# Kernel tuning notes

Measured on AMD Instinct MI355X. Metric: run time of the kernel, lower is better.

## Reference

```python
import jax, jax.numpy as jnp
import numpy as np

N_NODES = 100000
N_EDGES = 1600000
N_GRAPHS = 1024
IN_CH = 64
HID = 32
H4, H2 = HID * 4, HID * 2


def _glorot(key, shape):
    fan_in, fan_out = shape[0], shape[1]
    lim = (6.0 / (fan_in + fan_out)) ** 0.5
    return jax.random.uniform(key, shape, jnp.float32, -lim, lim)


def setup_inputs() -> dict:
    key = jax.random.key(0)
    ks = jax.random.split(key, 32)
    inp = {
        "x": jax.random.normal(ks[0], (N_NODES, IN_CH), jnp.float32),
        "edge_index": jax.random.randint(ks[1], (2, N_EDGES), 0, N_NODES, jnp.int64),
        "batch": jnp.sort(jax.random.randint(ks[2], (N_NODES,), 0, N_GRAPHS, jnp.int64)),
    }
    dims = [(IN_CH, H4), (H4, H2), (H2, H2), (H2, H2)]
    for i, (di, do) in enumerate(dims, 1):
        inp[f"c{i}_wl"] = _glorot(ks[3 * i], (di, do))
        inp[f"c{i}_bl"] = jnp.zeros((do,), jnp.float32)
        inp[f"c{i}_wr"] = _glorot(ks[3 * i + 1], (di, do))
    lin_dims = [(H2, H2), (H2, HID), (HID, HID), (HID, 1)]
    for i, (di, do) in enumerate(lin_dims, 1):
        inp[f"lin{i}_w"] = _glorot(ks[15 + 2 * i], (di, do))
        inp[f"lin{i}_b"] = jnp.zeros((do,), jnp.float32)
    return inp


def _sage(x, src, dst, wl, bl, wr):
    # mean-aggregate neighbor (source) features at target nodes
    agg = jax.ops.segment_sum(x[src], dst, num_segments=N_NODES)
    deg = jax.ops.segment_sum(jnp.ones((src.shape[0],), x.dtype), dst, num_segments=N_NODES)
    agg = agg / jnp.maximum(deg, 1.0)[:, None]
    return agg @ wl + bl + x @ wr


def reference(x, edge_index, batch,
              c1_wl, c1_bl, c1_wr, c2_wl, c2_bl, c2_wr,
              c3_wl, c3_bl, c3_wr, c4_wl, c4_bl, c4_wr,
              lin1_w, lin1_b, lin2_w, lin2_b, lin3_w, lin3_b, lin4_w, lin4_b):
    src, dst = edge_index[0], edge_index[1]
    h = jax.nn.relu(_sage(x, src, dst, c1_wl, c1_bl, c1_wr))
    h = jax.nn.relu(_sage(h, src, dst, c2_wl, c2_bl, c2_wr))
    h = jax.nn.relu(_sage(h, src, dst, c3_wl, c3_bl, c3_wr))
    h = jax.nn.relu(_sage(h, src, dst, c4_wl, c4_bl, c4_wr))
    # global mean pool over graphs
    gsum = jax.ops.segment_sum(h, batch, num_segments=N_GRAPHS)
    gcnt = jax.ops.segment_sum(jnp.ones((h.shape[0],), h.dtype), batch, num_segments=N_GRAPHS)
    g = gsum / jnp.maximum(gcnt, 1.0)[:, None]
    g = jax.nn.relu(g @ lin1_w + lin1_b)
    g = jax.nn.relu(g @ lin2_w + lin2_b)
    g = jax.nn.relu(g @ lin3_w + lin3_b)
    out = (g @ lin4_w + lin4_b).squeeze(1)  # [N_GRAPHS]
    return out
```

## Files before the change

### kernel.cpp

```cpp
#include <hip/hip_runtime.h>

#define NN 100000
#define NE 1600000
#define NG 1024
#define NBLK_SCAN ((NN + 255) / 256)
#define NPART 2
#define CPAD 4

#define GB_COUNT 6250
#define GB_Z     1563
#define GB_CVT   3125
#define GB_BND   5
#define GB_PREP  320
#define GB_SETUP (2 * GB_COUNT)

typedef __attribute__((ext_vector_type(8))) short bf16x8;
typedef __attribute__((ext_vector_type(4))) float f32x4;

__device__ __forceinline__ unsigned f2bf1(float f) {
  union { float f; unsigned u; } v; v.f = f;
  return (v.u + 0x7fffu + ((v.u >> 16) & 1u)) >> 16;
}
__device__ __forceinline__ unsigned packbf2(float a, float b) {
  return f2bf1(a) | (f2bf1(b) << 16);
}
__device__ __forceinline__ float bflo(unsigned u) {
  union { unsigned u; float f; } v; v.u = u << 16; return v.f;
}
__device__ __forceinline__ float bfhi(unsigned u) {
  union { unsigned u; float f; } v; v.u = u & 0xffff0000u; return v.f;
}
__device__ __forceinline__ float bfs(unsigned short s) {
  union { unsigned u; float f; } v; v.u = ((unsigned)s) << 16; return v.f;
}

__global__ __launch_bounds__(256) void k_prepz(const float* __restrict__ c1wr,
                                               unsigned short* __restrict__ pLZ) {
  int e = blockIdx.x * 256 + threadIdx.x;
  if (e >= 64 * 128) return;
  int k = e >> 7, n = e & 127;
  int t = k >> 5, kq = (k >> 3) & 3, j = k & 7;
  int n0 = n >> 4, nl = n & 15;
  pLZ[((((n0 * 2 + t) * 64) + (kq * 16 + nl)) << 3) + j] =
      (unsigned short)f2bf1(c1wr[k * 128 + n]);
}

__global__ __launch_bounds__(256) void k_setup(
    const int* __restrict__ dst, int* __restrict__ cnt, int* __restrict__ rank,
    const float* __restrict__ X, unsigned short* __restrict__ Xb,
    const int* __restrict__ batch, int* __restrict__ gstart,
    const unsigned short* __restrict__ pLZ, const float* __restrict__ c1bl,
    unsigned short* __restrict__ ZZ,
    const float* __restrict__ c1wl, const float* __restrict__ c1wr,
    const float* __restrict__ c2wl, const float* __restrict__ c2wr,
    const float* __restrict__ c3wl, const float* __restrict__ c3wr,
    const float* __restrict__ c4wl, const float* __restrict__ c4wr,
    unsigned short* __restrict__ pL1, unsigned short* __restrict__ pL2a,
    unsigned short* __restrict__ pL2b, unsigned short* __restrict__ pL3,
    unsigned short* __restrict__ pL4) {
  __shared__ __align__(16) char smem[64 * 66 * 4];
  int b = blockIdx.x, tid = threadIdx.x;

  if ((b & 1) == 0) {
    int e = (b >> 1) * 256 + tid;
    rank[e] = atomicAdd(&cnt[(size_t)dst[e] * CPAD], 1);
    return;
  }
  int ob = b >> 1;

  if (ob < GB_Z) {
    unsigned short* sA = (unsigned short*)smem;
    float* sC = (float*)smem;
    const int m0 = ob * 64;
#pragma unroll
    for (int l = 0; l < 2; ++l) {
      int c = tid + l * 256;
      int m = c >> 3, k8 = c & 7;
      int row = m0 + m;
      uint4 o = make_uint4(0, 0, 0, 0);
      if (row < NN) {
        const float4* xp = (const float4*)(X + (size_t)row * 64 + k8 * 8);
        float4 p0 = xp[0], p1 = xp[1];
        o.x = packbf2(p0.x, p0.y); o.y = packbf2(p0.z, p0.w);
        o.z = packbf2(p1.x, p1.y); o.w = packbf2(p1.z, p1.w);
      }
      int wv = m >> 4, mr = m & 15, t = k8 >> 2, kq = k8 & 3;
      ((uint4*)sA)[(wv * 2 + t) * 64 + kq * 16 + mr] = o;
    }
    __syncthreads();
    const int w = tid >> 6, L = tid & 63;
    const bf16x8* Af = (const bf16x8*)sA;
    const bf16x8* Bf = (const bf16x8*)pLZ;
    f32x4 acc[8];
#pragma unroll
    for (int i = 0; i < 8; ++i)
#pragma unroll
      for (int j = 0; j < 4; ++j) acc[i][j] = 0.f;
#pragma unroll
    for (int t = 0; t < 2; ++t) {
      bf16x8 afr = Af[(w * 2 + t) * 64 + L];
#pragma unroll
      for (int n0 = 0; n0 < 8; ++n0) {
        bf16x8 bfr = Bf[(n0 * 2 + t) * 64 + L];
        acc[n0] = __builtin_amdgcn_mfma_f32_16x16x32_bf16(afr, bfr, acc[n0], 0, 0, 0);
      }
    }
    int rg = L >> 4, cl = L & 15;
#pragma unroll
    for (int half = 0; half < 2; ++half) {
      __syncthreads();
#pragma unroll
      for (int n0 = 0; n0 < 4; ++n0)
#pragma unroll
        for (int r = 0; r < 4; ++r)
          sC[(w * 16 + rg * 4 + r) * 66 + n0 * 16 + cl] = acc[half * 4 + n0][r];
      __syncthreads();
#pragma unroll
      for (int it = 0; it < 2; ++it) {
        int c = tid + it * 256;
        int m = c >> 3, c8 = c & 7;
        int row = m0 + m;
        if (row < NN) {
          float v[8];
#pragma unroll
          for (int j = 0; j < 8; ++j)
            v[j] = sC[m * 66 + c8 * 8 + j] + c1bl[half * 64 + c8 * 8 + j];
          uint4 o;
          o.x = packbf2(v[0], v[1]); o.y = packbf2(v[2], v[3]);
          o.z = packbf2(v[4], v[5]); o.w = packbf2(v[6], v[7]);
          ((uint4*)(ZZ + (size_t)row * 128 + half * 64))[c8] = o;
        }
      }
    }
    return;
  }
  ob -= GB_Z;
  if (ob < GB_CVT) {
    int i = ob * 256 + tid;
    const float4* p = (const float4*)X + (size_t)i * 2;
    float4 a = p[0], c = p[1];
    uint4 o;
    o.x = packbf2(a.x, a.y); o.y = packbf2(a.z, a.w);
    o.z = packbf2(c.x, c.y); o.w = packbf2(c.z, c.w);
    ((uint4*)Xb)[i] = o;
    return;
  }
  ob -= GB_CVT;
  if (ob < GB_BND) {
    int g = ob * 256 + tid;
    if (g > NG) return;
    int lo = 0, hi = NN;
    while (lo < hi) {
      int mid = (lo + hi) >> 1;
      if (batch[mid] < g) lo = mid + 1; else hi = mid;
    }
    gstart[g] = lo;
    return;
  }
  ob -= GB_BND;
  if (ob < GB_PREP) {
    int yb = ob >> 6, xb = ob & 63;
    const float *WL, *WR; unsigned short* dstp; int N;
    if (yb == 0)      { WL = c1wl; WR = c1wr;           dstp = pL1;  N = 128; }
    else if (yb == 1) { WL = c2wl; WR = c2wl + 64 * 64; dstp = pL2a; N = 64; }
    else if (yb == 2) { WL = c2wr; WR = c2wr + 64 * 64; dstp = pL2b; N = 64; }
    else if (yb == 3) { WL = c3wl; WR = c3wr;           dstp = pL3;  N = 64; }
    else              { WL = c4wl; WR = c4wr;           dstp = pL4;  N = 64; }
    int e = xb * 256 + tid;
    if (e >= 128 * N) return;
    int k = e / N, n = e - k * N;
    float w = (k < 64) ? WL[k * N + n] : WR[(k - 64) * N + n];
    int t = k >> 5, kq = (k >> 3) & 3, j = k & 7;
    int n0 = n >> 4, nl = n & 15;
    dstp[((((n0 * 4 + t) * 64) + (kq * 16 + nl)) << 3) + j] =
        (unsigned short)f2bf1(w);
  }
}

__global__ __launch_bounds__(256) void k_scan1(const int* __restrict__ cnt,
                                               int* __restrict__ off,
                                               int* __restrict__ bsum) {
  __shared__ int s[256];
  int tid = threadIdx.x;
  int i = blockIdx.x * 256 + tid;
  int v = (i < NN) ? cnt[(size_t)i * CPAD] : 0;
  s[tid] = v;
  __syncthreads();
  for (int d = 1; d < 256; d <<= 1) {
    int t = (tid >= d) ? s[tid - d] : 0;
    __syncthreads();
    s[tid] += t;
    __syncthreads();
  }
  if (i < NN) off[i] = s[tid] - v;
  if (tid == 255) bsum[blockIdx.x] = s[255];
}

__global__ __launch_bounds__(256) void k_scan23(int* __restrict__ off,
                                                const int* __restrict__ bsum,
                                                const int* __restrict__ cnt,
                                                float* __restrict__ inv) {
  __shared__ int red[256];
  int b = blockIdx.x, tid = threadIdx.x;
  int s = 0;
  for (int j = tid; j < b; j += 256) s += bsum[j];
  red[tid] = s;
  __syncthreads();
  for (int d = 128; d > 0; d >>= 1) {
    if (tid < d) red[tid] += red[tid + d];
    __syncthreads();
  }
  int base = red[0];
  int i = b * 256 + tid;
  if (i < NN) {
    off[i] = off[i] + base;
    inv[i] = 1.0f / fmaxf((float)cnt[(size_t)i * CPAD], 1.0f);
  }
  if (i == 0) off[NN] = NE;
}

__global__ __launch_bounds__(256) void k_fill(const int* __restrict__ src,
                                              const int* __restrict__ dst,
                                              const int* __restrict__ off,
                                              const int* __restrict__ rank,
                                              int* __restrict__ csr) {
  int e = blockIdx.x * 256 + threadIdx.x;
  int lo = (int)blockIdx.y * (NN / NPART);
  int hi = lo + (NN / NPART);
  if (e < NE) {
    int d = dst[e];
    if (d >= lo && d < hi) csr[off[d] + rank[e]] = src[e];
  }
}

__global__ __launch_bounds__(256) void k_gather(
    const unsigned short* __restrict__ F, const int* __restrict__ csr,
    const int* __restrict__ off, const float* __restrict__ inv,
    const float* __restrict__ bias, const unsigned short* __restrict__ Z,
    unsigned short* __restrict__ out) {
  int idx = blockIdx.x * 256 + threadIdx.x;
  int n = idx >> 3, q = idx & 7;
  int beg = off[n], end = off[n + 1];
  float aA[8], aB[8];
#pragma unroll
  for (int c = 0; c < 8; ++c) { aA[c] = 0.f; aB[c] = 0.f; }
  int e = beg;
  for (; e + 4 <= end; e += 4) {
    uint4 v[4];
#pragma unroll
    for (int j = 0; j < 4; ++j)
      v[j] = ((const uint4*)(F + (size_t)csr[e + j] * 64))[q];
#pragma unroll
    for (int j = 0; j < 4; j += 2) {
      aA[0] += bflo(v[j].x); aB[0] += bflo(v[j + 1].x);
      aA[1] += bfhi(v[j].x); aB[1] += bfhi(v[j + 1].x);
      aA[2] += bflo(v[j].y); aB[2] += bflo(v[j + 1].y);
      aA[3] += bfhi(v[j].y); aB[3] += bfhi(v[j + 1].y);
      aA[4] += bflo(v[j].z); aB[4] += bflo(v[j + 1].z);
      aA[5] += bfhi(v[j].z); aB[5] += bfhi(v[j + 1].z);
      aA[6] += bflo(v[j].w); aB[6] += bflo(v[j + 1].w);
      aA[7] += bfhi(v[j].w); aB[7] += bfhi(v[j + 1].w);
    }
  }
  for (; e < end; ++e) {
    uint4 v0 = ((const uint4*)(F + (size_t)csr[e] * 64))[q];
    aA[0] += bflo(v0.x); aA[1] += bfhi(v0.x);
    aA[2] += bflo(v0.y); aA[3] += bfhi(v0.y);
    aA[4] += bflo(v0.z); aA[5] += bfhi(v0.z);
    aA[6] += bflo(v0.w); aA[7] += bfhi(v0.w);
  }
  float a[8];
  float iv = inv[n];
#pragma unroll
  for (int c = 0; c < 8; ++c) a[c] = (aA[c] + aB[c]) * iv;
  {
    uint4 z = ((const uint4*)(Z + (size_t)n * 64))[q];
    const float4* bp = (const float4*)(bias + q * 8);
    float4 b0 = bp[0], b1 = bp[1];
    a[0] = fmaxf(a[0] + b0.x + bflo(z.x), 0.f);
    a[1] = fmaxf(a[1] + b0.y + bfhi(z.x), 0.f);
    a[2] = fmaxf(a[2] + b0.z + bflo(z.y), 0.f);
    a[3] = fmaxf(a[3] + b0.w + bfhi(z.y), 0.f);
    a[4] = fmaxf(a[4] + b1.x + bflo(z.z), 0.f);
    a[5] = fmaxf(a[5] + b1.y + bfhi(z.z), 0.f);
    a[6] = fmaxf(a[6] + b1.z + bflo(z.w), 0.f);
    a[7] = fmaxf(a[7] + b1.w + bfhi(z.w), 0.f);
  }
  uint4 o;
  o.x = packbf2(a[0], a[1]); o.y = packbf2(a[2], a[3]);
  o.z = packbf2(a[4], a[5]); o.w = packbf2(a[6], a[7]);
  ((uint4*)(out + (size_t)n * 64))[q] = o;
}

__global__ __launch_bounds__(256, 4) void k_fgemm1(
    const unsigned short* __restrict__ F, const int* __restrict__ csr,
    const int* __restrict__ off, const float* __restrict__ inv,
    const unsigned short* __restrict__ Wp,
    const unsigned short* __restrict__ ZZ,
    unsigned short* __restrict__ OUT) {
  __shared__ __align__(16) char smem[64 * 66 * 4];
  unsigned short* sA = (unsigned short*)smem;
  float* sC = (float*)smem;
  const int tid = threadIdx.x;
  const int m0 = blockIdx.x * 64;

  {
    int m = tid >> 2, qr = tid & 3;
    int row = m0 + m;
    float a0[16], a1[16];
#pragma unroll
    for (int c = 0; c < 16; ++c) { a0[c] = 0.f; a1[c] = 0.f; }
    if (row < NN) {
      int beg = off[row], end = off[row + 1];
      int e = beg;
      for (; e + 2 <= end; e += 2) {
        int s0 = csr[e], s1 = csr[e + 1];
        const uint4* r0 = (const uint4*)(F + (size_t)s0 * 64) + qr * 2;
        const uint4* r1 = (const uint4*)(F + (size_t)s1 * 64) + qr * 2;
        uint4 p0 = r0[0], p1 = r0[1], q0 = r1[0], q1 = r1[1];
        a0[0] += bflo(p0.x); a0[1] += bfhi(p0.x);
        a0[2] += bflo(p0.y); a0[3] += bfhi(p0.y);
        a0[4] += bflo(p0.z); a0[5] += bfhi(p0.z);
        a0[6] += bflo(p0.w); a0[7] += bfhi(p0.w);
        a0[8] += bflo(p1.x); a0[9] += bfhi(p1.x);
        a0[10] += bflo(p1.y); a0[11] += bfhi(p1.y);
        a0[12] += bflo(p1.z); a0[13] += bfhi(p1.z);
        a0[14] += bflo(p1.w); a0[15] += bfhi(p1.w);
        a1[0] += bflo(q0.x); a1[1] += bfhi(q0.x);
        a1[2] += bflo(q0.y); a1[3] += bfhi(q0.y);
        a1[4] += bflo(q0.z); a1[5] += bfhi(q0.z);
        a1[6] += bflo(q0.w); a1[7] += bfhi(q0.w);
        a1[8] += bflo(q1.x); a1[9] += bfhi(q1.x);
        a1[10] += bflo(q1.y); a1[11] += bfhi(q1.y);
        a1[12] += bflo(q1.z); a1[13] += bfhi(q1.z);
        a1[14] += bflo(q1.w); a1[15] += bfhi(q1.w);
      }
      if (e < end) {
        const uint4* r0 = (const uint4*)(F + (size_t)csr[e] * 64) + qr * 2;
        uint4 p0 = r0[0], p1 = r0[1];
        a0[0] += bflo(p0.x); a0[1] += bfhi(p0.x);
        a0[2] += bflo(p0.y); a0[3] += bfhi(p0.y);
        a0[4] += bflo(p0.z); a0[5] += bfhi(p0.z);
        a0[6] += bflo(p0.w); a0[7] += bfhi(p0.w);
        a0[8] += bflo(p1.x); a0[9] += bfhi(p1.x);
        a0[10] += bflo(p1.y); a0[11] += bfhi(p1.y);
        a0[12] += bflo(p1.z); a0[13] += bfhi(p1.z);
        a0[14] += bflo(p1.w); a0[15] += bfhi(p1.w);
      }
      float iv = inv[row];
#pragma unroll
      for (int c = 0; c < 16; ++c) a0[c] = (a0[c] + a1[c]) * iv;
    }
    int wv = m >> 4, mr = m & 15;
#pragma unroll
    for (int h = 0; h < 2; ++h) {
      int k8 = qr * 2 + h;
      int t = k8 >> 2, kq = k8 & 3;
      uint4 o;
      o.x = packbf2(a0[h * 8 + 0], a0[h * 8 + 1]);
      o.y = packbf2(a0[h * 8 + 2], a0[h * 8 + 3]);
      o.z = packbf2(a0[h * 8 + 4], a0[h * 8 + 5]);
      o.w = packbf2(a0[h * 8 + 6], a0[h * 8 + 7]);
      ((uint4*)sA)[(wv * 2 + t) * 64 + kq * 16 + mr] = o;
    }
  }
  __syncthreads();

  const int w = tid >> 6, L = tid & 63;
  const bf16x8* Af = (const bf16x8*)sA;
  const bf16x8* Bf = (const bf16x8*)Wp;
  f32x4 acc[8];
#pragma unroll
  for (int i = 0; i < 8; ++i)
#pragma unroll
    for (int j = 0; j < 4; ++j) acc[i][j] = 0.f;
#pragma unroll
  for (int t = 0; t < 2; ++t) {
    bf16x8 afr = Af[(w * 2 + t) * 64 + L];
#pragma unroll
    for (int n0 = 0; n0 < 8; ++n0) {
      bf16x8 bfr = Bf[(n0 * 4 + t) * 64 + L];
      acc[n0] = __builtin_amdgcn_mfma_f32_16x16x32_bf16(afr, bfr, acc[n0], 0, 0, 0);
    }
  }

  int rg = L >> 4, cl = L & 15;
#pragma unroll
  for (int half = 0; half < 2; ++half) {
    __syncthreads();
#pragma unroll
    for (int n0 = 0; n0 < 4; ++n0)
#pragma unroll
      for (int r = 0; r < 4; ++r)
        sC[(w * 16 + rg * 4 + r) * 66 + n0 * 16 + cl] = acc[half * 4 + n0][r];
    __syncthreads();
#pragma unroll
    for (int it = 0; it < 2; ++it) {
      int c = tid + it * 256;
      int m = c >> 3, c8 = c & 7;
      int row = m0 + m;
      if (row < NN) {
        uint4 z = ((const uint4*)(ZZ + (size_t)row * 128 + half * 64))[c8];
        float zb[8] = {bflo(z.x), bfhi(z.x), bflo(z.y), bfhi(z.y),
                       bflo(z.z), bfhi(z.z), bflo(z.w), bfhi(z.w)};
        float v[8];
#pragma unroll
        for (int j = 0; j < 8; ++j)
          v[j] = fmaxf(sC[m * 66 + c8 * 8 + j] + zb[j], 0.f);
        uint4 o;
        o.x = packbf2(v[0], v[1]); o.y = packbf2(v[2], v[3]);
        o.z = packbf2(v[4], v[5]); o.w = packbf2(v[6], v[7]);
        ((uint4*)(OUT + (size_t)row * 128 + half * 64))[c8] = o;
      }
    }
  }
}

template <int NF>
__global__ __launch_bounds__(256, 4) void k_fgemm(
    const unsigned short* __restrict__ F, const int* __restrict__ csr,
    const int* __restrict__ off, const float* __restrict__ inv,
    const unsigned short* __restrict__ Wp, const float* __restrict__ bias,
    unsigned short* __restrict__ OUT, int outStride) {
  __shared__ __align__(16) char smem[64 * 66 * 4];
  unsigned short* sA = (unsigned short*)smem;
  float* sC = (float*)smem;
  const int tid = threadIdx.x;
  const int m0 = blockIdx.x * 64;

  {
    int m = tid >> 2, qr = tid & 3;
    int row = m0 + m;
    float a0[16], a1[16];
#pragma unroll
    for (int c = 0; c < 16; ++c) { a0[c] = 0.f; a1[c] = 0.f; }
    if (row < NN) {
      int beg = off[row], end = off[row + 1];
      int e = beg;
      for (; e + 2 <= end; e += 2) {
        int s0 = csr[e], s1 = csr[e + 1];
        const uint4* r0 = (const uint4*)(F + (size_t)s0 * 64) + qr * 2;
        const uint4* r1 = (const uint4*)(F + (size_t)s1 * 64) + qr * 2;
        uint4 p0 = r0[0], p1 = r0[1], q0 = r1[0], q1 = r1[1];
        a0[0] += bflo(p0.x); a0[1] += bfhi(p0.x);
        a0[2] += bflo(p0.y); a0[3] += bfhi(p0.y);
        a0[4] += bflo(p0.z); a0[5] += bfhi(p0.z);
        a0[6] += bflo(p0.w); a0[7] += bfhi(p0.w);
        a0[8] += bflo(p1.x); a0[9] += bfhi(p1.x);
        a0[10] += bflo(p1.y); a0[11] += bfhi(p1.y);
        a0[12] += bflo(p1.z); a0[13] += bfhi(p1.z);
        a0[14] += bflo(p1.w); a0[15] += bfhi(p1.w);
        a1[0] += bflo(q0.x); a1[1] += bfhi(q0.x);
        a1[2] += bflo(q0.y); a1[3] += bfhi(q0.y);
        a1[4] += bflo(q0.z); a1[5] += bfhi(q0.z);
        a1[6] += bflo(q0.w); a1[7] += bfhi(q0.w);
        a1[8] += bflo(q1.x); a1[9] += bfhi(q1.x);
        a1[10] += bflo(q1.y); a1[11] += bfhi(q1.y);
        a1[12] += bflo(q1.z); a1[13] += bfhi(q1.z);
        a1[14] += bflo(q1.w); a1[15] += bfhi(q1.w);
      }
      if (e < end) {
        const uint4* r0 = (const uint4*)(F + (size_t)csr[e] * 64) + qr * 2;
        uint4 p0 = r0[0], p1 = r0[1];
        a0[0] += bflo(p0.x); a0[1] += bfhi(p0.x);
        a0[2] += bflo(p0.y); a0[3] += bfhi(p0.y);
        a0[4] += bflo(p0.z); a0[5] += bfhi(p0.z);
        a0[6] += bflo(p0.w); a0[7] += bfhi(p0.w);
        a0[8] += bflo(p1.x); a0[9] += bfhi(p1.x);
        a0[10] += bflo(p1.y); a0[11] += bfhi(p1.y);
        a0[12] += bflo(p1.z); a0[13] += bfhi(p1.z);
        a0[14] += bflo(p1.w); a0[15] += bfhi(p1.w);
      }
      float iv = inv[row];
#pragma unroll
      for (int c = 0; c < 16; ++c) a0[c] = (a0[c] + a1[c]) * iv;
    }
    int wv = m >> 4, mr = m & 15;
#pragma unroll
    for (int h = 0; h < 2; ++h) {
      int k8 = qr * 2 + h;
      int t = k8 >> 2, kq = k8 & 3;
      uint4 o;
      o.x = packbf2(a0[h * 8 + 0], a0[h * 8 + 1]);
      o.y = packbf2(a0[h * 8 + 2], a0[h * 8 + 3]);
      o.z = packbf2(a0[h * 8 + 4], a0[h * 8 + 5]);
      o.w = packbf2(a0[h * 8 + 6], a0[h * 8 + 7]);
      ((uint4*)sA)[(wv * 4 + t) * 64 + kq * 16 + mr] = o;
    }
  }
#pragma unroll
  for (int l = 0; l < 2; ++l) {
    int c = tid + l * 256;
    int m = c >> 3, j = c & 7;
    int row = m0 + m;
    uint4 v = make_uint4(0, 0, 0, 0);
    if (row < NN) v = ((const uint4*)(F + (size_t)row * 64))[j];
    int k8 = 8 + j, t = k8 >> 2, kq = k8 & 3;
    int wv = m >> 4, mr = m & 15;
    ((uint4*)sA)[(wv * 4 + t) * 64 + kq * 16 + mr] = v;
  }
  __syncthreads();

  const int w = tid >> 6, L = tid & 63;
  const bf16x8* Af = (const bf16x8*)sA;
  const bf16x8* Bf = (const bf16x8*)Wp;
  f32x4 acc[NF];
#pragma unroll
  for (int i = 0; i < NF; ++i)
#pragma unroll
    for (int j = 0; j < 4; ++j) acc[i][j] = 0.f;
#pragma unroll
  for (int t = 0; t < 4; ++t) {
    bf16x8 afr = Af[(w * 4 + t) * 64 + L];
#pragma unroll
    for (int n0 = 0; n0 < NF; ++n0) {
      bf16x8 bfr = Bf[(n0 * 4 + t) * 64 + L];
      acc[n0] = __builtin_amdgcn_mfma_f32_16x16x32_bf16(afr, bfr, acc[n0], 0, 0, 0);
    }
  }

  int rg = L >> 4, cl = L & 15;
#pragma unroll
  for (int half = 0; half < NF / 4; ++half) {
    __syncthreads();
#pragma unroll
    for (int n0 = 0; n0 < 4; ++n0)
#pragma unroll
      for (int r = 0; r < 4; ++r)
        sC[(w * 16 + rg * 4 + r) * 66 + n0 * 16 + cl] = acc[half * 4 + n0][r];
    __syncthreads();
#pragma unroll
    for (int it = 0; it < 2; ++it) {
      int c = tid + it * 256;
      int m = c >> 3, c8 = c & 7;
      int row = m0 + m;
      if (row < NN) {
        float v[8];
#pragma unroll
        for (int j = 0; j < 8; ++j)
          v[j] = fmaxf(sC[m * 66 + c8 * 8 + j] + bias[half * 64 + c8 * 8 + j], 0.f);
        uint4 o;
        o.x = packbf2(v[0], v[1]); o.y = packbf2(v[2], v[3]);
        o.z = packbf2(v[4], v[5]); o.w = packbf2(v[6], v[7]);
        ((uint4*)(OUT + (size_t)row * outStride + half * 64))[c8] = o;
      }
    }
  }
}

__global__ __launch_bounds__(256) void k_gemm(
    const unsigned short* __restrict__ S0,
    const unsigned short* __restrict__ Wp,
    const unsigned short* __restrict__ Wp2, unsigned short* __restrict__ OUT2,
    unsigned short* __restrict__ OUT, int M) {
  __shared__ __align__(16) char smem[64 * 66 * 4];
  unsigned short* sA = (unsigned short*)smem;
  float* sC = (float*)smem;
  const int tid = threadIdx.x;
  if (blockIdx.y == 1) { Wp = Wp2; OUT = OUT2; }
  const int m0 = blockIdx.x * 64;

#pragma unroll
  for (int l = 0; l < 4; ++l) {
    int c = tid + l * 256;
    int m = c >> 4, k8 = c & 15;
    int row = m0 + m;
    uint4 v = make_uint4(0, 0, 0, 0);
    if (row < M) v = ((const uint4*)(S0 + (size_t)row * 128))[k8];
    int wv = m >> 4, mr = m & 15, t = k8 >> 2, kq = k8 & 3;
    ((uint4*)sA)[(wv * 4 + t) * 64 + (kq * 16 + mr)] = v;
  }
  __syncthreads();

  const int w = tid >> 6, L = tid & 63;
  f32x4 acc[4];
#pragma unroll
  for (int i = 0; i < 4; ++i)
#pragma unroll
    for (int j = 0; j < 4; ++j) acc[i][j] = 0.f;

  const bf16x8* Af = (const bf16x8*)sA;
  const bf16x8* Bf = (const bf16x8*)Wp;
#pragma unroll
  for (int t = 0; t < 4; ++t) {
    bf16x8 afr = Af[(w * 4 + t) * 64 + L];
#pragma unroll
    for (int n0 = 0; n0 < 4; ++n0) {
      bf16x8 bfr = Bf[(n0 * 4 + t) * 64 + L];
      acc[n0] = __builtin_amdgcn_mfma_f32_16x16x32_bf16(afr, bfr, acc[n0], 0, 0, 0);
    }
  }
  __syncthreads();
  {
    int rg = L >> 4, cl = L & 15;
#pragma unroll
    for (int n0 = 0; n0 < 4; ++n0)
#pragma unroll
      for (int r = 0; r < 4; ++r)
        sC[(w * 16 + rg * 4 + r) * 66 + n0 * 16 + cl] = acc[n0][r];
  }
  __syncthreads();
#pragma unroll
  for (int it = 0; it < 2; ++it) {
    int c = tid + it * 256;
    int m = c >> 3, c8 = c & 7;
    int row = m0 + m;
    if (row < M) {
      float v[8];
#pragma unroll
      for (int j = 0; j < 8; ++j) v[j] = sC[m * 66 + c8 * 8 + j];
      uint4 o;
      o.x = packbf2(v[0], v[1]); o.y = packbf2(v[2], v[3]);
      o.z = packbf2(v[4], v[5]); o.w = packbf2(v[6], v[7]);
      ((uint4*)(OUT + (size_t)row * 64))[c8] = o;
    }
  }
}

__global__ __launch_bounds__(64) void k_poolmlp(
    const unsigned short* __restrict__ H, const int* __restrict__ gstart,
    const float* __restrict__ w1, const float* __restrict__ b1,
    const float* __restrict__ w2, const float* __restrict__ b2,
    const float* __restrict__ w3, const float* __restrict__ b3,
    const float* __restrict__ w4, const float* __restrict__ b4,
    float* __restrict__ out) {
  __shared__ float sg[64], s1[64], s2[32], s3[32];
  int g = blockIdx.x, t = threadIdx.x;
  int beg = gstart[g], end = gstart[g + 1];
  float acc = 0.0f;
#pragma unroll 4
  for (int n = beg; n < end; ++n) acc += bfs(H[(size_t)n * 64 + t]);
  float cnt = fmaxf((float)(end - beg), 1.0f);
  sg[t] = acc / cnt;
  __syncthreads();
  acc = b1[t];
  for (int k = 0; k < 64; ++k) acc += sg[k] * w1[k * 64 + t];
  s1[t] = fmaxf(acc, 0.0f);
  __syncthreads();
  if (t < 32) {
    acc = b2[t];
    for (int k = 0; k < 64; ++k) acc += s1[k] * w2[k * 32 + t];
    s2[t] = fmaxf(acc, 0.0f);
  }
  __syncthreads();
  if (t < 32) {
    acc = b3[t];
    for (int k = 0; k < 32; ++k) acc += s2[k] * w3[k * 32 + t];
    s3[t] = fmaxf(acc, 0.0f);
  }
  __syncthreads();
  if (t == 0) {
    acc = b4[0];
    for (int k = 0; k < 32; ++k) acc += s3[k] * w4[k];
    out[g] = acc;
  }
}

extern "C" void kernel_launch(void* const* d_in, const int* in_sizes, int n_in,
                              void* d_out, int out_size, void* d_ws,
                              size_t ws_size, hipStream_t stream) {
  const float* x     = (const float*)d_in[0];
  const int*   ei    = (const int*)d_in[1];
  const int*   batch = (const int*)d_in[2];
  const int* src = ei;
  const int* dst = ei + NE;

  const float* c1_wl = (const float*)d_in[3];
  const float* c1_bl = (const float*)d_in[4];
  const float* c1_wr = (const float*)d_in[5];
  const float* c2_wl = (const float*)d_in[6];
  const float* c2_bl = (const float*)d_in[7];
  const float* c2_wr = (const float*)d_in[8];
  const float* c3_wl = (const float*)d_in[9];
  const float* c3_bl = (const float*)d_in[10];
  const float* c3_wr = (const float*)d_in[11];
  const float* c4_wl = (const float*)d_in[12];
  const float* c4_bl = (const float*)d_in[13];
  const float* c4_wr = (const float*)d_in[14];
  const float* l1w = (const float*)d_in[15];
  const float* l1b = (const float*)d_in[16];
  const float* l2w = (const float*)d_in[17];
  const float* l2b = (const float*)d_in[18];
  const float* l3w = (const float*)d_in[19];
  const float* l3b = (const float*)d_in[20];
  const float* l4w = (const float*)d_in[21];
  const float* l4b = (const float*)d_in[22];

  char* wsb = (char*)d_ws;
  float* inv = (float*)wsb;
  unsigned short* xb  = (unsigned short*)(wsb + (size_t)NN * 4);
  unsigned short* B1  = xb + (size_t)NN * 64;
  unsigned short* B2  = B1 + (size_t)NN * 64;
  unsigned short* B3  = B2 + (size_t)NN * 128;
  unsigned short* B4  = B3 + (size_t)NN * 64;
  unsigned short* ZZ  = B4 + (size_t)NN * 64;
  unsigned short* pL1  = ZZ + (size_t)NN * 128;
  unsigned short* pL2a = pL1 + 128 * 128;
  unsigned short* pL2b = pL2a + 128 * 64;
  unsigned short* pL3  = pL2b + 128 * 64;
  unsigned short* pL4  = pL3 + 128 * 64;
  unsigned short* pLZ  = pL4 + 128 * 64;
  int* cnt    = (int*)(pLZ + 64 * 128);
  int* off    = cnt + (size_t)NN * CPAD;
  int* bsum   = off + NN + 1;
  int* gstart = bsum + 512;
  int* csr    = gstart + NG + 1 + 2;
  int* rank   = csr + NE;

  const int gE  = (NE + 255) / 256;
  const int gN8 = NN * 8 / 256;
  const int gM  = (NN + 63) / 64;
  const int gN  = NBLK_SCAN;

  hipMemsetAsync(cnt, 0, (size_t)NN * CPAD * 4, stream);

  k_prepz<<<32, 256, 0, stream>>>(c1_wr, pLZ);

  k_setup<<<GB_SETUP, 256, 0, stream>>>(dst, cnt, rank, x, xb, batch, gstart,
                                        pLZ, c1_bl, ZZ,
                                        c1_wl, c1_wr, c2_wl, c2_wr,
                                        c3_wl, c3_wr, c4_wl, c4_wr,
                                        pL1, pL2a, pL2b, pL3, pL4);
  k_scan1<<<gN, 256, 0, stream>>>(cnt, off, bsum);
  k_scan23<<<gN, 256, 0, stream>>>(off, bsum, cnt, inv);
  k_fill<<<dim3(gE, NPART), 256, 0, stream>>>(src, dst, off, rank, csr);

  k_fgemm1<<<gM, 256, 0, stream>>>(xb, csr, off, inv, pL1, ZZ, B2);

  k_gemm<<<dim3(gM, 2), 256, 0, stream>>>(B2, pL2a, pL2b, B4, B3, NN);
  k_gather<<<gN8, 256, 0, stream>>>(B3, csr, off, inv, c2_bl, B4, B1);

  k_fgemm<4><<<gM, 256, 0, stream>>>(B1, csr, off, inv, pL3, c3_bl, B3, 64);

  k_fgemm<4><<<gM, 256, 0, stream>>>(B3, csr, off, inv, pL4, c4_bl, B1, 64);

  k_poolmlp<<<NG, 64, 0, stream>>>(B1, gstart, l1w, l1b, l2w, l2b,
                                   l3w, l3b, l4w, l4b, (float*)d_out);
}
```

Measured before the change: 402.0 us.

## Fuse scan into single-pass decoupled lookback; merge memset and weight prep; unsplit fill

Replaces the two-kernel prefix scan with a single-pass scan that uses decoupled lookback over per-block descriptors, and computes inv from the already-loaded count. The hipMemsetAsync and the pLZ prep kernel are merged into one kernel that also zeroes the descriptors. k_fill no longer partitions destinations into two passes. The goal is fewer launches and less redundant traffic. The lookback relies on blocks being scheduled in order for forward progress, and the unpartitioned fill loses whatever locality the split gave.

```diff
diff --git a/kernel.cpp b/kernel.cpp
--- a/kernel.cpp
+++ b/kernel.cpp
@@ -4,7 +4,6 @@
 #define NE 1600000
 #define NG 1024
 #define NBLK_SCAN ((NN + 255) / 256)
-#define NPART 2
 #define CPAD 4
 
 #define GB_COUNT 6250
@@ -14,6 +13,8 @@
 #define GB_PREP  320
 #define GB_SETUP (2 * GB_COUNT)
 
+#define GB_P0 (32 + (NN * CPAD + 255) / 256)
+
 typedef __attribute__((ext_vector_type(8))) short bf16x8;
 typedef __attribute__((ext_vector_type(4))) float f32x4;
 
@@ -34,15 +35,25 @@
   union { unsigned u; float f; } v; v.u = ((unsigned)s) << 16; return v.f;
 }
 
-__global__ __launch_bounds__(256) void k_prepz(const float* __restrict__ c1wr,
-                                               unsigned short* __restrict__ pLZ) {
-  int e = blockIdx.x * 256 + threadIdx.x;
-  if (e >= 64 * 128) return;
-  int k = e >> 7, n = e & 127;
-  int t = k >> 5, kq = (k >> 3) & 3, j = k & 7;
-  int n0 = n >> 4, nl = n & 15;
-  pLZ[((((n0 * 2 + t) * 64) + (kq * 16 + nl)) << 3) + j] =
-      (unsigned short)f2bf1(c1wr[k * 128 + n]);
+__global__ __launch_bounds__(256) void k_prep0(const float* __restrict__ c1wr,
+                                               unsigned short* __restrict__ pLZ,
+                                               int* __restrict__ cnt,
+                                               unsigned long long* __restrict__ desc) {
+  int b = blockIdx.x, tid = threadIdx.x;
+  if (b < 32) {
+    int e = b * 256 + tid;
+    if (e < 64 * 128) {
+      int k = e >> 7, n = e & 127;
+      int t = k >> 5, kq = (k >> 3) & 3, j = k & 7;
+      int n0 = n >> 4, nl = n & 15;
+      pLZ[((((n0 * 2 + t) * 64) + (kq * 16 + nl)) << 3) + j] =
+          (unsigned short)f2bf1(c1wr[k * 128 + n]);
+    }
+    return;
+  }
+  if (b == 32) { desc[tid] = 0ULL; desc[tid + 256] = 0ULL; }
+  int i = (b - 32) * 256 + tid;
+  if (i < NN * CPAD) cnt[i] = 0;
 }
 
 __global__ __launch_bounds__(256) void k_setup(
@@ -177,12 +188,14 @@
   }
 }
 
-__global__ __launch_bounds__(256) void k_scan1(const int* __restrict__ cnt,
-                                               int* __restrict__ off,
-                                               int* __restrict__ bsum) {
+__global__ __launch_bounds__(256) void k_scan(const int* __restrict__ cnt,
+                                              int* __restrict__ off,
+                                              float* __restrict__ inv,
+                                              unsigned long long* __restrict__ desc) {
   __shared__ int s[256];
-  int tid = threadIdx.x;
-  int i = blockIdx.x * 256 + tid;
+  __shared__ int sbase;
+  int b = blockIdx.x, tid = threadIdx.x;
+  int i = b * 256 + tid;
   int v = (i < NN) ? cnt[(size_t)i * CPAD] : 0;
   s[tid] = v;
   __syncthreads();
@@ -192,29 +205,25 @@
     s[tid] += t;
     __syncthreads();
   }
-  if (i < NN) off[i] = s[tid] - v;
-  if (tid == 255) bsum[blockIdx.x] = s[255];
-}
-
-__global__ __launch_bounds__(256) void k_scan23(int* __restrict__ off,
-                                                const int* __restrict__ bsum,
-                                                const int* __restrict__ cnt,
-                                                float* __restrict__ inv) {
-  __shared__ int red[256];
-  int b = blockIdx.x, tid = threadIdx.x;
-  int s = 0;
-  for (int j = tid; j < b; j += 256) s += bsum[j];
-  red[tid] = s;
-  __syncthreads();
-  for (int d = 128; d > 0; d >>= 1) {
-    if (tid < d) red[tid] += red[tid + d];
-    __syncthreads();
-  }
-  int base = red[0];
-  int i = b * 256 + tid;
+  if (tid == 0) {
+    unsigned long long total = (unsigned long long)s[255];
+    atomicExch(&desc[b], (total << 2) | 1ULL);
+    long long base = 0;
+    int j = b - 1;
+    while (j >= 0) {
+      unsigned long long d2;
+      do { d2 = atomicAdd(&desc[j], 0ULL); } while ((d2 & 3ULL) == 0ULL);
+      base += (long long)(d2 >> 2);
+      if ((d2 & 3ULL) == 2ULL) break;
+      --j;
+    }
+    atomicExch(&desc[b], (((unsigned long long)(base + (long long)total)) << 2) | 2ULL);
+    sbase = (int)base;
+  }
+  __syncthreads();
   if (i < NN) {
-    off[i] = off[i] + base;
-    inv[i] = 1.0f / fmaxf((float)cnt[(size_t)i * CPAD], 1.0f);
+    off[i] = sbase + s[tid] - v;
+    inv[i] = 1.0f / fmaxf((float)v, 1.0f);
   }
   if (i == 0) off[NN] = NE;
 }
@@ -225,12 +234,7 @@
                                               const int* __restrict__ rank,
                                               int* __restrict__ csr) {
   int e = blockIdx.x * 256 + threadIdx.x;
-  int lo = (int)blockIdx.y * (NN / NPART);
-  int hi = lo + (NN / NPART);
-  if (e < NE) {
-    int d = dst[e];
-    if (d >= lo && d < hi) csr[off[d] + rank[e]] = src[e];
-  }
+  if (e < NE) csr[off[dst[e]] + rank[e]] = src[e];
 }
 
 __global__ __launch_bounds__(256) void k_gather(
@@ -702,28 +706,26 @@
   unsigned short* pLZ  = pL4 + 128 * 64;
   int* cnt    = (int*)(pLZ + 64 * 128);
   int* off    = cnt + (size_t)NN * CPAD;
-  int* bsum   = off + NN + 1;
-  int* gstart = bsum + 512;
+  int* gstart = off + NN + 1;
   int* csr    = gstart + NG + 1 + 2;
   int* rank   = csr + NE;
+  unsigned long long* desc =
+      (unsigned long long*)(((uintptr_t)(rank + NE) + 15) & ~(uintptr_t)15);
 
   const int gE  = (NE + 255) / 256;
   const int gN8 = NN * 8 / 256;
   const int gM  = (NN + 63) / 64;
   const int gN  = NBLK_SCAN;
 
-  hipMemsetAsync(cnt, 0, (size_t)NN * CPAD * 4, stream);
-
-  k_prepz<<<32, 256, 0, stream>>>(c1_wr, pLZ);
+  k_prep0<<<GB_P0, 256, 0, stream>>>(c1_wr, pLZ, cnt, desc);
 
   k_setup<<<GB_SETUP, 256, 0, stream>>>(dst, cnt, rank, x, xb, batch, gstart,
                                         pLZ, c1_bl, ZZ,
                                         c1_wl, c1_wr, c2_wl, c2_wr,
                                         c3_wl, c3_wr, c4_wl, c4_wr,
                                         pL1, pL2a, pL2b, pL3, pL4);
-  k_scan1<<<gN, 256, 0, stream>>>(cnt, off, bsum);
-  k_scan23<<<gN, 256, 0, stream>>>(off, bsum, cnt, inv);
-  k_fill<<<dim3(gE, NPART), 256, 0, stream>>>(src, dst, off, rank, csr);
+  k_scan<<<gN, 256, 0, stream>>>(cnt, off, inv, desc);
+  k_fill<<<gE, 256, 0, stream>>>(src, dst, off, rank, csr);
 
   k_fgemm1<<<gM, 256, 0, stream>>>(xb, csr, off, inv, pL1, ZZ, B2);
 
```

After: 407.3 us. No clear change (+1.3%).
